# Optimization experiments

Hardware: AMD Instinct MI355X
Metric: run time of the kernel (lower is better)

The kernel has to match this reference:

```python
import jax, jax.numpy as jnp
import numpy as np

B, N, D = 4, 4096, 256
H = 4
HD = D // H
FF = max(2 * D, 16)
EPS = 1e-5


def layer_norm(x, w, b):
    mu = jnp.mean(x, axis=-1, keepdims=True)
    var = jnp.mean(jnp.square(x - mu), axis=-1, keepdims=True)
    return (x - mu) * jax.lax.rsqrt(var + EPS) * w + b


def setup_inputs() -> dict:
    key = jax.random.key(0)
    ks = jax.random.split(key, 12)
    s = 1.0 / np.sqrt(D)
    sf = 1.0 / np.sqrt(FF)
    return {
        "tokens": jax.random.normal(ks[0], (B, N, D), jnp.float32),
        "importance": jax.random.normal(ks[1], (B, N), jnp.float32),
        "norm1_w": jnp.ones((D,), jnp.float32),
        "norm1_b": jnp.zeros((D,), jnp.float32),
        "Wq": jax.random.uniform(ks[2], (D, D), jnp.float32, -s, s),
        "bq": jnp.zeros((D,), jnp.float32),
        "Wk": jax.random.uniform(ks[3], (D, D), jnp.float32, -s, s),
        "bk": jnp.zeros((D,), jnp.float32),
        "Wv": jax.random.uniform(ks[4], (D, D), jnp.float32, -s, s),
        "bv": jnp.zeros((D,), jnp.float32),
        "Wo": jax.random.uniform(ks[5], (D, D), jnp.float32, -s, s),
        "bo": jnp.zeros((D,), jnp.float32),
        "norm2_w": jnp.ones((D,), jnp.float32),
        "norm2_b": jnp.zeros((D,), jnp.float32),
        "W1": jax.random.uniform(ks[6], (D, FF), jnp.float32, -s, s),
        "b1": jnp.zeros((FF,), jnp.float32),
        "W2": jax.random.uniform(ks[7], (FF, D), jnp.float32, -sf, sf),
        "b2": jnp.zeros((D,), jnp.float32),
    }


def reference(tokens, importance, norm1_w, norm1_b, Wq, bq, Wk, bk, Wv, bv,
              Wo, bo, norm2_w, norm2_b, W1, b1, W2, b2):
    # pre-norm MHA with additive importance bias
    x = layer_norm(tokens, norm1_w, norm1_b)
    q = (x @ Wq + bq).reshape(B, N, H, HD).transpose(0, 2, 1, 3)  # [B,H,N,HD]
    k = (x @ Wk + bk).reshape(B, N, H, HD).transpose(0, 2, 1, 3)
    v = (x @ Wv + bv).reshape(B, N, H, HD).transpose(0, 2, 1, 3)
    scores = jnp.einsum("bhnd,bhmd->bhnm", q, k) / np.sqrt(HD)
    scores = scores + importance[:, None, None, :]  # bias over key dim
    attn = jax.nn.softmax(scores, axis=-1)
    ctx = jnp.einsum("bhnm,bhmd->bhnd", attn, v)
    ctx = ctx.transpose(0, 2, 1, 3).reshape(B, N, D)
    x = tokens + (ctx @ Wo + bo)
    # GELU FFN (exact erf gelu, matching torch default)
    y = layer_norm(x, norm2_w, norm2_b)
    y = jax.nn.gelu(y @ W1 + b1, approximate=False) @ W2 + b2
    return x + y
```

## Files before the change

### kernel.cpp

```cpp
#include <hip/hip_runtime.h>

#define Bb 4
#define Nn 4096
#define Dd 256
#define Hh 4
#define HDd 64
#define FFf 512
#define MT 16384

typedef __attribute__((ext_vector_type(8))) short short8;
typedef __attribute__((ext_vector_type(4))) float f32x4;
typedef __attribute__((ext_vector_type(16))) float f32x16;
typedef unsigned short u16;
typedef unsigned int u32;
typedef __attribute__((ext_vector_type(4))) u32 u32x4;

typedef __attribute__((address_space(1))) const void glb_src;
typedef __attribute__((address_space(3))) void lds_dst;

__device__ __forceinline__ void gload_lds16(const void* g, void* l) {
    __builtin_amdgcn_global_load_lds((glb_src*)g, (lds_dst*)l, 16, 0, 0);
}

__device__ __forceinline__ u16 f2bf(float f) {
    union { float f; u32 i; } v; v.f = f;
    u32 r = v.i + 0x7FFFu + ((v.i >> 16) & 1u);
    return (u16)(r >> 16);
}

__device__ __forceinline__ short8 ld8(const u16* p) {
    return *(const short8*)p;
}

__device__ __forceinline__ void pl32swap(u32& a, u32& b) {
    asm("v_permlane32_swap_b32 %0, %1" : "+v"(a), "+v"(b));
}
__device__ __forceinline__ float xhalf_max(float x) {
    u32 a = __float_as_uint(x), b = a;
    pl32swap(a, b);
    return fmaxf(__uint_as_float(a), __uint_as_float(b));
}
__device__ __forceinline__ u32 cvtpk(float lo, float hi) {
    u32 r;
    asm("v_cvt_pk_bf16_f32 %0, %1, %2" : "=v"(r) : "v"(lo), "v"(hi));
    return r;
}
__device__ __forceinline__ float fexp2(float x) {
    float r;
    asm("v_exp_f32 %0, %1" : "=v"(r) : "v"(x));
    return r;
}
__device__ __forceinline__ float max3f(float a, float b, float c) {
    float r;
    asm("v_max3_f32 %0, %1, %2, %3" : "=v"(r) : "v"(a), "v"(b), "v"(c));
    return r;
}

#define QSCALE 0.18033610062f
#define LOG2E  1.44269504089f

__global__ __launch_bounds__(256) void prep_kernel(
        const float* __restrict__ Wq, const float* __restrict__ Wk,
        const float* __restrict__ Wv, const float* __restrict__ Wo,
        const float* __restrict__ W1, const float* __restrict__ W2,
        const float* __restrict__ imp,
        u16* __restrict__ WqkvT, u16* __restrict__ WoT,
        u16* __restrict__ W1T, u16* __restrict__ W2T,
        u32* __restrict__ impPk) {
    int e = blockIdx.x * 256 + threadIdx.x;
    if (e < 196608) {
        int c = e >> 8, k = e & 255;
        int mat = c >> 8;
        int cc = c & 255;
        const float* W = (mat == 0) ? Wq : ((mat == 1) ? Wk : Wv);
        WqkvT[(size_t)c * 256 + k] = f2bf(W[k * 256 + cc]);
    } else if (e < 262144) {
        int i = e - 196608; int n = i >> 8, k = i & 255;
        WoT[n * 256 + k] = f2bf(Wo[k * 256 + n]);
    } else if (e < 393216) {
        int i = e - 262144; int n = i >> 8, k = i & 255;
        W1T[n * 256 + k] = f2bf(W1[k * 512 + n]);
    } else if (e < 524288) {
        int i = e - 393216; int n = i >> 9, k = i & 511;
        W2T[n * 512 + k] = f2bf(W2[k * 256 + n]);
    } else {
        int i = e - 524288;
        float ivs = imp[i] * LOG2E;
        u16 ih = f2bf(ivs);
        float rem = ivs - __uint_as_float(((u32)ih) << 16);
        u16 il = f2bf(rem);
        impPk[i] = ((u32)il << 16) | ih;
    }
}

__global__ __launch_bounds__(256) void ln_kernel(const float* __restrict__ x,
        const float* __restrict__ w, const float* __restrict__ bia,
        u16* __restrict__ out) {
    int lane = threadIdx.x & 63;
    int row = blockIdx.x * 4 + (threadIdx.x >> 6);
    const float* xr = x + (size_t)row * Dd;
    float4 v = *(const float4*)(xr + lane * 4);
    float s = v.x + v.y + v.z + v.w;
    float s2 = v.x * v.x + v.y * v.y + v.z * v.z + v.w * v.w;
    #pragma unroll
    for (int off = 1; off < 64; off <<= 1) {
        s  += __shfl_xor(s, off);
        s2 += __shfl_xor(s2, off);
    }
    float mu = s * (1.0f / Dd);
    float var = s2 * (1.0f / Dd) - mu * mu;
    float rstd = rsqrtf(var + 1e-5f);
    float4 wv = *(const float4*)(w + lane * 4);
    float4 bv = *(const float4*)(bia + lane * 4);
    ushort4 ov;
    ov.x = f2bf((v.x - mu) * rstd * wv.x + bv.x);
    ov.y = f2bf((v.y - mu) * rstd * wv.y + bv.y);
    ov.z = f2bf((v.z - mu) * rstd * wv.z + bv.z);
    ov.w = f2bf((v.w - mu) * rstd * wv.w + bv.w);
    *(ushort4*)(out + (size_t)row * Dd + lane * 4) = ov;
}

template<int MODE, int KD, int BM>
__global__ __launch_bounds__(256) void gemm_bt(
        const u16* __restrict__ A, const u16* __restrict__ BT,
        const float* __restrict__ bias0, const float* __restrict__ bias1,
        const float* __restrict__ bias2,
        const float* __restrict__ resid, float* __restrict__ outf,
        u16* __restrict__ o0, u16* __restrict__ o1, u16* __restrict__ o2) {
    constexpr int AM = BM / 32;
    __shared__ u16 Asl[BM * 32];
    __shared__ u16 Bsl[128 * 32];
    int lane = threadIdx.x & 63;
    int wv = threadIdx.x >> 6;
    int wm = wv >> 1, wn = wv & 1;
    int m0 = blockIdx.y * BM, n0 = blockIdx.x * 128;
    f32x4 zz; zz[0] = 0.f; zz[1] = 0.f; zz[2] = 0.f; zz[3] = 0.f;
    f32x4 acc[AM][4];
    #pragma unroll
    for (int i = 0; i < AM; ++i)
        #pragma unroll
        for (int j = 0; j < 4; ++j) acc[i][j] = zz;

    for (int kt = 0; kt < KD; kt += 32) {
        __syncthreads();
        #pragma unroll
        for (int i = 0; i < BM / 64; ++i) {
            int chunk = threadIdx.x + i * 256;
            int row = chunk >> 2, c16 = chunk & 3;
            int srcc = (c16 ^ (row & 3)) * 8;
            gload_lds16(A + (size_t)(m0 + row) * KD + kt + srcc,
                        (char*)Asl + wv * 1024 + i * 4096);
        }
        #pragma unroll
        for (int i = 0; i < 2; ++i) {
            int chunk = threadIdx.x + i * 256;
            int row = chunk >> 2, c16 = chunk & 3;
            int srcc = (c16 ^ (row & 3)) * 8;
            gload_lds16(BT + (size_t)(n0 + row) * KD + kt + srcc,
                        (char*)Bsl + wv * 1024 + i * 4096);
        }
        __syncthreads();
        short8 af[AM], bfr[4];
        #pragma unroll
        for (int t = 0; t < AM; ++t) {
            int arow = wm * (BM / 2) + t * 16 + (lane & 15);
            af[t] = ld8(Asl + arow * 32 + (((lane >> 4) * 8) ^ ((arow & 3) * 8)));
        }
        #pragma unroll
        for (int t = 0; t < 4; ++t) {
            int brow = wn * 64 + t * 16 + (lane & 15);
            bfr[t] = ld8(Bsl + brow * 32 + (((lane >> 4) * 8) ^ ((brow & 3) * 8)));
        }
        #pragma unroll
        for (int mt = 0; mt < AM; ++mt)
            #pragma unroll
            for (int nt = 0; nt < 4; ++nt)
                acc[mt][nt] = __builtin_amdgcn_mfma_f32_16x16x32_bf16(af[mt], bfr[nt], acc[mt][nt], 0, 0, 0);
    }

    #pragma unroll
    for (int mt = 0; mt < AM; ++mt) {
        #pragma unroll
        for (int nt = 0; nt < 4; ++nt) {
            #pragma unroll
            for (int r = 0; r < 4; ++r) {
                int row = m0 + wm * (BM / 2) + mt * 16 + (lane >> 4) * 4 + r;
                int col = n0 + wn * 64 + nt * 16 + (lane & 15);
                float v = acc[mt][nt][r];
                if (MODE == 0) {
                    int mat = col >> 8;
                    int cc = col & 255;
                    int hh = cc >> 6, dd = cc & 63;
                    int bbi = row >> 12, nni = row & 4095;
                    int bh = bbi * Hh + hh;
                    if (mat == 0)      o0[((size_t)bh * Nn + nni) * HDd + dd] = f2bf((v + bias0[cc]) * QSCALE);
                    else if (mat == 1) o1[((size_t)bh * Nn + nni) * HDd + dd] = f2bf(v + bias1[cc]);
                    else               o2[((size_t)bh * HDd + dd) * Nn + nni] = f2bf(v + bias2[cc]);
                } else if (MODE == 1) {
                    outf[(size_t)row * Dd + col] = resid[(size_t)row * Dd + col] + v + bias0[col];
                } else if (MODE == 2) {
                    float xg = v + bias0[col];
                    float g = 0.5f * xg * (1.0f + erff(xg * 0.70710678118654752f));
                    o0[(size_t)row * FFf + col] = f2bf(g);
                } else {
                    outf[(size_t)row * Dd + col] = resid[(size_t)row * Dd + col] + v + bias0[col];
                }
            }
        }
    }
}

__global__ __launch_bounds__(256, 4) void attn_kernel(
        const u16* __restrict__ Qb, const u16* __restrict__ Kb,
        const u16* __restrict__ VTb, const u32* __restrict__ impPk,
        u16* __restrict__ pc, float* __restrict__ pm, float* __restrict__ pl) {
    __shared__ u16 Klds[2][64 * 64];
    __shared__ u16 Vlds[2][64 * 64];
    int lane = threadIdx.x & 63;
    int wv = threadIdx.x >> 6;
    int kvh = blockIdx.x >> 9;
    int bh = (blockIdx.x >> 5) & 15;
    int qt = blockIdx.x & 31;
    int bbi = bh >> 2;
    int qrow0 = qt * 128 + wv * 32;
    int q = lane & 31;
    int hf = lane >> 5;
    int key0 = kvh * 2048;
    int pg = kvh * 16 + bh;

    short8 qf[4];
    #pragma unroll
    for (int ks = 0; ks < 4; ++ks)
        qf[ks] = ld8(Qb + ((size_t)bh * Nn + qrow0 + q) * HDd + ks * 16 + hf * 8);

    short8 onef = (short8)0;
    if (hf == 0) { onef[0] = (short)0x3F80; onef[1] = (short)0x3F80; }
    short8 aone;
    #pragma unroll
    for (int j = 0; j < 8; ++j) aone[j] = (short)0x3F80;

    int sr = lane >> 3;
    int sc = lane & 7;
    int swz = (sc ^ sr) * 8;
    const u16* kp = Kb + ((size_t)bh * Nn + key0 + wv * 16 + sr) * HDd + swz;
    const u16* vp = VTb + ((size_t)bh * HDd + wv * 16 + sr) * Nn + key0 + swz;
    size_t ib = (size_t)bbi * Nn;

    gload_lds16(kp,           (char*)Klds[0] + wv * 2048);
    gload_lds16(kp + 8 * HDd, (char*)Klds[0] + wv * 2048 + 1024);
    gload_lds16(vp,           (char*)Vlds[0] + wv * 2048);
    gload_lds16(vp + 8 * Nn,  (char*)Vlds[0] + wv * 2048 + 1024);
    kp += 64 * HDd; vp += 64;
    u32 npk0 = impPk[ib + key0 + q], npk1 = impPk[ib + key0 + 32 + q];

    f32x16 ctx[2], lacc;
    #pragma unroll
    for (int r = 0; r < 16; ++r) { ctx[0][r] = 0.f; ctx[1][r] = 0.f; lacc[r] = 0.f; }
    float m = -__builtin_inff();

    int cur = 0;
    for (int t = 0; t < 32; ++t) {
        __syncthreads();
        u32 pk0 = npk0, pk1 = npk1;
        if (t < 31) {
            gload_lds16(kp,           (char*)Klds[cur ^ 1] + wv * 2048);
            gload_lds16(kp + 8 * HDd, (char*)Klds[cur ^ 1] + wv * 2048 + 1024);
            gload_lds16(vp,           (char*)Vlds[cur ^ 1] + wv * 2048);
            gload_lds16(vp + 8 * Nn,  (char*)Vlds[cur ^ 1] + wv * 2048 + 1024);
            kp += 64 * HDd; vp += 64;
            npk0 = impPk[ib + key0 + t * 64 + 64 + q];
            npk1 = impPk[ib + key0 + t * 64 + 96 + q];
        }
        const u16* Kc = Klds[cur];
        const u16* Vc = Vlds[cur];

        f32x16 s0, s1;
        #pragma unroll
        for (int r = 0; r < 16; ++r) { s0[r] = 0.f; s1[r] = 0.f; }
        __builtin_amdgcn_s_setprio(1);
        #pragma unroll
        for (int ks = 0; ks < 4; ++ks) {
            short8 kf0 = ld8(Kc + q * 64 + (((ks * 2 + hf) ^ (q & 7)) * 8));
            short8 kf1 = ld8(Kc + (32 + q) * 64 + (((ks * 2 + hf) ^ (q & 7)) * 8));
            s0 = __builtin_amdgcn_mfma_f32_32x32x16_bf16(kf0, qf[ks], s0, 0, 0, 0);
            s1 = __builtin_amdgcn_mfma_f32_32x32x16_bf16(kf1, qf[ks], s1, 0, 0, 0);
        }
        short8 af0 = (short8)0, af1 = (short8)0;
        if (hf == 0) {
            af0[0] = (short)(pk0 & 0xFFFFu); af0[1] = (short)(pk0 >> 16);
            af1[0] = (short)(pk1 & 0xFFFFu); af1[1] = (short)(pk1 >> 16);
        }
        s0 = __builtin_amdgcn_mfma_f32_32x32x16_bf16(af0, onef, s0, 0, 0, 0);
        s1 = __builtin_amdgcn_mfma_f32_32x32x16_bf16(af1, onef, s1, 0, 0, 0);
        __builtin_amdgcn_s_setprio(0);

        float a0 = max3f(s0[0], s0[1], s0[2]);
        float a1 = max3f(s0[3], s0[4], s0[5]);
        float a2 = max3f(s0[6], s0[7], s0[8]);
        float a3 = max3f(s0[9], s0[10], s0[11]);
        float a4 = max3f(s0[12], s0[13], s0[14]);
        float b0 = max3f(s1[0], s1[1], s1[2]);
        float b1 = max3f(s1[3], s1[4], s1[5]);
        float b2 = max3f(s1[6], s1[7], s1[8]);
        float b3 = max3f(s1[9], s1[10], s1[11]);
        float b4 = max3f(s1[12], s1[13], s1[14]);
        float c0 = max3f(a0, a1, a2);
        float c1 = max3f(a3, a4, s0[15]);
        float c2 = max3f(b0, b1, b2);
        float c3 = max3f(b3, b4, s1[15]);
        float tm = fmaxf(max3f(c0, c1, c2), c3);
        tm = xhalf_max(tm);
        bool nore = __all(tm <= m + 8.0f);
        if (!nore) {
            float nm = fmaxf(m, tm);
            float al = fexp2(m - nm);
            lacc[0] *= al;
            #pragma unroll
            for (int r = 0; r < 16; ++r) { ctx[0][r] *= al; ctx[1][r] *= al; }
            m = nm;
        }
        #pragma unroll
        for (int r = 0; r < 16; ++r) { s0[r] = fexp2(s0[r] - m); s1[r] = fexp2(s1[r] - m); }

        u32 w0[8], w1[8];
        #pragma unroll
        for (int j = 0; j < 8; ++j) {
            w0[j] = cvtpk(s0[2 * j], s0[2 * j + 1]);
            w1[j] = cvtpk(s1[2 * j], s1[2 * j + 1]);
        }
        pl32swap(w0[0], w0[2]); pl32swap(w0[1], w0[3]);
        pl32swap(w0[4], w0[6]); pl32swap(w0[5], w0[7]);
        pl32swap(w1[0], w1[2]); pl32swap(w1[1], w1[3]);
        pl32swap(w1[4], w1[6]); pl32swap(w1[5], w1[7]);
        u32x4 t00; t00[0] = w0[0]; t00[1] = w0[1]; t00[2] = w0[2]; t00[3] = w0[3];
        u32x4 t01; t01[0] = w0[4]; t01[1] = w0[5]; t01[2] = w0[6]; t01[3] = w0[7];
        u32x4 t10; t10[0] = w1[0]; t10[1] = w1[1]; t10[2] = w1[2]; t10[3] = w1[3];
        u32x4 t11; t11[0] = w1[4]; t11[1] = w1[5]; t11[2] = w1[6]; t11[3] = w1[7];
        short8 pf00 = __builtin_bit_cast(short8, t00);
        short8 pf01 = __builtin_bit_cast(short8, t01);
        short8 pf10 = __builtin_bit_cast(short8, t10);
        short8 pf11 = __builtin_bit_cast(short8, t11);

        __builtin_amdgcn_s_setprio(1);
        lacc = __builtin_amdgcn_mfma_f32_32x32x16_bf16(aone, pf00, lacc, 0, 0, 0);
        lacc = __builtin_amdgcn_mfma_f32_32x32x16_bf16(aone, pf01, lacc, 0, 0, 0);
        lacc = __builtin_amdgcn_mfma_f32_32x32x16_bf16(aone, pf10, lacc, 0, 0, 0);
        lacc = __builtin_amdgcn_mfma_f32_32x32x16_bf16(aone, pf11, lacc, 0, 0, 0);
        #pragma unroll
        for (int dt = 0; dt < 2; ++dt) {
            int vrow = dt * 32 + q;
            const u16* vb = Vc + vrow * 64;
            int sw = vrow & 7;
            short8 vf;
            vf = ld8(vb + (((0 + hf) ^ sw) * 8));
            ctx[dt] = __builtin_amdgcn_mfma_f32_32x32x16_bf16(vf, pf00, ctx[dt], 0, 0, 0);
            vf = ld8(vb + (((2 + hf) ^ sw) * 8));
            ctx[dt] = __builtin_amdgcn_mfma_f32_32x32x16_bf16(vf, pf01, ctx[dt], 0, 0, 0);
            vf = ld8(vb + (((4 + hf) ^ sw) * 8));
            ctx[dt] = __builtin_amdgcn_mfma_f32_32x32x16_bf16(vf, pf10, ctx[dt], 0, 0, 0);
            vf = ld8(vb + (((6 + hf) ^ sw) * 8));
            ctx[dt] = __builtin_amdgcn_mfma_f32_32x32x16_bf16(vf, pf11, ctx[dt], 0, 0, 0);
        }
        __builtin_amdgcn_s_setprio(0);
        cur ^= 1;
    }

    int qg = qrow0 + q;
    if (hf == 0) {
        pm[(size_t)pg * Nn + qg] = m;
        pl[(size_t)pg * Nn + qg] = lacc[0];
    }
    #pragma unroll
    for (int dt = 0; dt < 2; ++dt) {
        #pragma unroll
        for (int r = 0; r < 16; ++r) {
            int d = dt * 32 + (r & 3) + 8 * (r >> 2) + 4 * hf;
            pc[((size_t)pg * 64 + d) * Nn + qg] = f2bf(ctx[dt][r]);
        }
    }
}

__global__ __launch_bounds__(256) void merge_kernel(
        const u16* __restrict__ pc, const float* __restrict__ pm,
        const float* __restrict__ pl, u16* __restrict__ ctxOut) {
    __shared__ float trans[64][65];
    __shared__ float f0a[64], f1a[64];
    int bh = blockIdx.x >> 6;
    int q0 = (blockIdx.x & 63) * 64;
    int t = threadIdx.x;
    if (t < 64) {
        int qg = q0 + t;
        float m0 = pm[(size_t)bh * Nn + qg];
        float m1 = pm[(size_t)(16 + bh) * Nn + qg];
        float l0 = pl[(size_t)bh * Nn + qg];
        float l1 = pl[(size_t)(16 + bh) * Nn + qg];
        float M = fmaxf(m0, m1);
        float w0 = fexp2(m0 - M), w1 = fexp2(m1 - M);
        float inv = 1.0f / (l0 * w0 + l1 * w1);
        f0a[t] = w0 * inv; f1a[t] = w1 * inv;
    }
    __syncthreads();
    int wv = t >> 6, lane = t & 63;
    #pragma unroll
    for (int i = 0; i < 16; ++i) {
        int d = wv * 16 + i;
        float c0 = __uint_as_float((u32)pc[((size_t)bh * 64 + d) * Nn + q0 + lane] << 16);
        float c1 = __uint_as_float((u32)pc[((size_t)(16 + bh) * 64 + d) * Nn + q0 + lane] << 16);
        trans[lane][d] = c0 * f0a[lane] + c1 * f1a[lane];
    }
    __syncthreads();
    int q = t >> 2, dg = t & 3;
    int b = bh >> 2, h = bh & 3;
    const float* tr = &trans[q][dg * 16];
    uint4 pa, pb;
    pa.x = cvtpk(tr[0], tr[1]);  pa.y = cvtpk(tr[2], tr[3]);
    pa.z = cvtpk(tr[4], tr[5]);  pa.w = cvtpk(tr[6], tr[7]);
    pb.x = cvtpk(tr[8], tr[9]);  pb.y = cvtpk(tr[10], tr[11]);
    pb.z = cvtpk(tr[12], tr[13]); pb.w = cvtpk(tr[14], tr[15]);
    u16* op = ctxOut + ((size_t)b * Nn + q0 + q) * Dd + h * 64 + dg * 16;
    *(uint4*)op = pa;
    *(uint4*)(op + 8) = pb;
}

extern "C" void kernel_launch(void* const* d_in, const int* in_sizes, int n_in,
                              void* d_out, int out_size, void* d_ws, size_t ws_size,
                              hipStream_t stream) {
    (void)in_sizes; (void)n_in; (void)out_size; (void)ws_size;
    const float* tokens     = (const float*)d_in[0];
    const float* importance = (const float*)d_in[1];
    const float* n1w = (const float*)d_in[2];
    const float* n1b = (const float*)d_in[3];
    const float* Wq  = (const float*)d_in[4];
    const float* bq  = (const float*)d_in[5];
    const float* Wk  = (const float*)d_in[6];
    const float* bk  = (const float*)d_in[7];
    const float* Wv  = (const float*)d_in[8];
    const float* bv  = (const float*)d_in[9];
    const float* Wo  = (const float*)d_in[10];
    const float* bo  = (const float*)d_in[11];
    const float* n2w = (const float*)d_in[12];
    const float* n2b = (const float*)d_in[13];
    const float* W1  = (const float*)d_in[14];
    const float* b1  = (const float*)d_in[15];
    const float* W2  = (const float*)d_in[16];
    const float* b2  = (const float*)d_in[17];
    float* out = (float*)d_out;

    char* ws = (char*)d_ws;
    const size_t MB = (size_t)1 << 20;
    u16* xln   = (u16*)(ws);
    u16* qb    = (u16*)(ws + 8 * MB);
    u16* kb    = (u16*)(ws + 16 * MB);
    u16* vT    = (u16*)(ws + 24 * MB);
    u16* ctx   = (u16*)(ws + 32 * MB);
    u16* pc    = (u16*)(ws + 40 * MB);
    float* pm  = (float*)(ws + 56 * MB);
    float* pl  = (float*)(ws + 56 * MB + 524288);
    u16* WqkvT = (u16*)(ws + 57 * MB);
    u16* WoT   = (u16*)(ws + 57 * MB + 393216);
    u16* W1T   = (u16*)(ws + 57 * MB + 393216 + 131072);
    u16* W2T   = (u16*)(ws + 57 * MB + 393216 + 131072 + 262144);
    u32* impPk = (u32*)(ws + 57 * MB + 393216 + 131072 + 262144 + 262144);
    u16* yln   = xln;
    u16* hbuf  = qb;
    float* x2  = out;

    prep_kernel<<<2112, 256, 0, stream>>>(Wq, Wk, Wv, Wo, W1, W2, importance,
                                          WqkvT, WoT, W1T, W2T, impPk);
    ln_kernel<<<4096, 256, 0, stream>>>(tokens, n1w, n1b, xln);
    gemm_bt<0, 256, 128><<<dim3(6, 128), 256, 0, stream>>>(xln, WqkvT, bq, bk, bv,
                                                           nullptr, nullptr, qb, kb, vT);
    attn_kernel<<<1024, 256, 0, stream>>>(qb, kb, vT, impPk, pc, pm, pl);
    merge_kernel<<<1024, 256, 0, stream>>>(pc, pm, pl, ctx);
    gemm_bt<1, 256, 64><<<dim3(2, 256), 256, 0, stream>>>(ctx, WoT, bo, nullptr, nullptr,
                                                          tokens, x2, nullptr, nullptr, nullptr);
    ln_kernel<<<4096, 256, 0, stream>>>(x2, n2w, n2b, yln);
    gemm_bt<2, 256, 64><<<dim3(4, 256), 256, 0, stream>>>(yln, W1T, b1, nullptr, nullptr,
                                                          nullptr, nullptr, hbuf, nullptr, nullptr);
    gemm_bt<3, 512, 64><<<dim3(2, 256), 256, 0, stream>>>(hbuf, W2T, b2, nullptr, nullptr,
                                                          x2, out, nullptr, nullptr, nullptr);
}
```

Measured before the change: 200.4 us.

## Fuse output projection with residual add and second LayerNorm

Replaces the Wo GEMM and the separate LayerNorm launch with one kernel. Each block computes a full 32-row by 256-column tile, adds bias and residual, stages the rows in LDS, then computes LayerNorm and writes bf16 normalized rows. This removes one launch and a re-read of x2. In exchange it uses a single-buffered K loop, a one-pass variance formula, and a smaller per-block tile that loads the full weight matrix for every block.

```diff
diff --git a/kernel.cpp b/kernel.cpp
--- a/kernel.cpp
+++ b/kernel.cpp
@@ -196,8 +196,6 @@
                     if (mat == 0)      o0[((size_t)bh * Nn + nni) * HDd + dd] = f2bf((v + bias0[cc]) * QSCALE);
                     else if (mat == 1) o1[((size_t)bh * Nn + nni) * HDd + dd] = f2bf(v + bias1[cc]);
                     else               o2[((size_t)bh * HDd + dd) * Nn + nni] = f2bf(v + bias2[cc]);
-                } else if (MODE == 1) {
-                    outf[(size_t)row * Dd + col] = resid[(size_t)row * Dd + col] + v + bias0[col];
                 } else if (MODE == 2) {
                     float xg = v + bias0[col];
                     float g = 0.5f * xg * (1.0f + erff(xg * 0.70710678118654752f));
@@ -207,6 +205,110 @@
                 }
             }
         }
+    }
+}
+
+__global__ __launch_bounds__(256) void oproj_ln_kernel(
+        const u16* __restrict__ A, const u16* __restrict__ BT,
+        const float* __restrict__ bias, const float* __restrict__ resid,
+        const float* __restrict__ lnw, const float* __restrict__ lnb,
+        float* __restrict__ x2, u16* __restrict__ yln) {
+    __shared__ u16 Asl[32 * 32];
+    __shared__ u16 Bsl[256 * 32];
+    __shared__ float xlds[32][256];
+    int lane = threadIdx.x & 63;
+    int wv = threadIdx.x >> 6;
+    int m0 = blockIdx.x * 32;
+    f32x4 zz; zz[0] = 0.f; zz[1] = 0.f; zz[2] = 0.f; zz[3] = 0.f;
+    f32x4 acc[2][4];
+    #pragma unroll
+    for (int i = 0; i < 2; ++i)
+        #pragma unroll
+        for (int j = 0; j < 4; ++j) acc[i][j] = zz;
+
+    for (int kt = 0; kt < Dd; kt += 32) {
+        __syncthreads();
+        if (wv < 2) {
+            int t = threadIdx.x;
+            int row = t >> 2, c16 = t & 3;
+            int srcc = (c16 ^ (row & 3)) * 8;
+            gload_lds16(A + (size_t)(m0 + row) * Dd + kt + srcc,
+                        (char*)Asl + wv * 1024);
+        }
+        #pragma unroll
+        for (int i = 0; i < 4; ++i) {
+            int chunk = threadIdx.x + i * 256;
+            int row = chunk >> 2, c16 = chunk & 3;
+            int srcc = (c16 ^ (row & 3)) * 8;
+            gload_lds16(BT + (size_t)row * Dd + kt + srcc,
+                        (char*)Bsl + wv * 1024 + i * 4096);
+        }
+        __syncthreads();
+        short8 af[2], bfr[4];
+        #pragma unroll
+        for (int t = 0; t < 2; ++t) {
+            int arow = t * 16 + (lane & 15);
+            af[t] = ld8(Asl + arow * 32 + (((lane >> 4) * 8) ^ ((arow & 3) * 8)));
+        }
+        #pragma unroll
+        for (int t = 0; t < 4; ++t) {
+            int brow = wv * 64 + t * 16 + (lane & 15);
+            bfr[t] = ld8(Bsl + brow * 32 + (((lane >> 4) * 8) ^ ((brow & 3) * 8)));
+        }
+        #pragma unroll
+        for (int mt = 0; mt < 2; ++mt)
+            #pragma unroll
+            for (int nt = 0; nt < 4; ++nt)
+                acc[mt][nt] = __builtin_amdgcn_mfma_f32_16x16x32_bf16(af[mt], bfr[nt], acc[mt][nt], 0, 0, 0);
+    }
+
+    #pragma unroll
+    for (int mt = 0; mt < 2; ++mt) {
+        #pragma unroll
+        for (int nt = 0; nt < 4; ++nt) {
+            #pragma unroll
+            for (int r = 0; r < 4; ++r) {
+                int row = mt * 16 + (lane >> 4) * 4 + r;
+                int col = wv * 64 + nt * 16 + (lane & 15);
+                float v = resid[(size_t)(m0 + row) * Dd + col] + acc[mt][nt][r] + bias[col];
+                x2[(size_t)(m0 + row) * Dd + col] = v;
+                xlds[row][col] = v;
+            }
+        }
+    }
+    __syncthreads();
+
+    int rw = threadIdx.x >> 3;
+    int cg = (threadIdx.x & 7) * 32;
+    float s = 0.f, s2 = 0.f;
+    #pragma unroll
+    for (int j = 0; j < 32; ++j) {
+        float v = xlds[rw][cg + j];
+        s += v; s2 += v * v;
+    }
+    #pragma unroll
+    for (int off = 1; off < 8; off <<= 1) {
+        s  += __shfl_xor(s, off);
+        s2 += __shfl_xor(s2, off);
+    }
+    float mu = s * (1.0f / Dd);
+    float var = s2 * (1.0f / Dd) - mu * mu;
+    float rstd = rsqrtf(var + 1e-5f);
+    u16* op = yln + (size_t)(m0 + rw) * Dd + cg;
+    #pragma unroll
+    for (int j = 0; j < 32; j += 8) {
+        float v0 = (xlds[rw][cg + j + 0] - mu) * rstd * lnw[cg + j + 0] + lnb[cg + j + 0];
+        float v1 = (xlds[rw][cg + j + 1] - mu) * rstd * lnw[cg + j + 1] + lnb[cg + j + 1];
+        float v2 = (xlds[rw][cg + j + 2] - mu) * rstd * lnw[cg + j + 2] + lnb[cg + j + 2];
+        float v3 = (xlds[rw][cg + j + 3] - mu) * rstd * lnw[cg + j + 3] + lnb[cg + j + 3];
+        float v4 = (xlds[rw][cg + j + 4] - mu) * rstd * lnw[cg + j + 4] + lnb[cg + j + 4];
+        float v5 = (xlds[rw][cg + j + 5] - mu) * rstd * lnw[cg + j + 5] + lnb[cg + j + 5];
+        float v6 = (xlds[rw][cg + j + 6] - mu) * rstd * lnw[cg + j + 6] + lnb[cg + j + 6];
+        float v7 = (xlds[rw][cg + j + 7] - mu) * rstd * lnw[cg + j + 7] + lnb[cg + j + 7];
+        uint4 pk;
+        pk.x = cvtpk(v0, v1); pk.y = cvtpk(v2, v3);
+        pk.z = cvtpk(v4, v5); pk.w = cvtpk(v6, v7);
+        *(uint4*)(op + j) = pk;
     }
 }
 
@@ -472,9 +574,7 @@
                                                            nullptr, nullptr, qb, kb, vT);
     attn_kernel<<<1024, 256, 0, stream>>>(qb, kb, vT, impPk, pc, pm, pl);
     merge_kernel<<<1024, 256, 0, stream>>>(pc, pm, pl, ctx);
-    gemm_bt<1, 256, 64><<<dim3(2, 256), 256, 0, stream>>>(ctx, WoT, bo, nullptr, nullptr,
-                                                          tokens, x2, nullptr, nullptr, nullptr);
-    ln_kernel<<<4096, 256, 0, stream>>>(x2, n2w, n2b, yln);
+    oproj_ln_kernel<<<512, 256, 0, stream>>>(ctx, WoT, bo, tokens, n2w, n2b, x2, yln);
     gemm_bt<2, 256, 64><<<dim3(4, 256), 256, 0, stream>>>(yln, W1T, b1, nullptr, nullptr,
                                                           nullptr, nullptr, hbuf, nullptr, nullptr);
     gemm_bt<3, 512, 64><<<dim3(2, 256), 256, 0, stream>>>(hbuf, W2T, b2, nullptr, nullptr,
```

Result: no change. 197.0 us (-1.7%).
